# Kernel tuning notes

Hardware: AMD Instinct MI355X
Metric: run time of the kernel (lower is better)

The kernel has to match this reference:

```python
import jax, jax.numpy as jnp
import numpy as np
from jax import lax

NUM_INITS = 64
MODEL_MODE = ['conv', 'conv', 'dense']
SIZE_ARRAY = [(16, 1, 5, 5), (16,), (32, 16, 5, 5), (32,), (10, 512), (10,)]
_flat = [int(np.prod(s)) for s in SIZE_ARRAY]
BP = np.concatenate(([0], np.cumsum(_flat)))  # breakpoints into flat param vector
TOTAL_PARAMS = int(BP[-1])  # 18378
BATCH_N = 128


def setup_inputs() -> dict:
    key = jax.random.key(0)
    k1, k2 = jax.random.split(key)
    params = jax.random.normal(k1, (NUM_INITS, TOTAL_PARAMS), dtype=jnp.float32) * 0.05
    batch = jax.random.normal(k2, (BATCH_N, 1, 28, 28), dtype=jnp.float32)
    return {"params": params, "batch": batch}


def _conv_relu_pool(x, w, b):
    # x: (N, C_in, H, W), w: (C_out, C_in, k, k), b: (C_out,)
    y = lax.conv_general_dilated(x, w, window_strides=(1, 1), padding='VALID',
                                 dimension_numbers=('NCHW', 'OIHW', 'NCHW'))
    y = jax.nn.relu(y + b[None, :, None, None])
    # MaxPool2d(2, 2) over spatial dims
    return lax.reduce_window(y, -jnp.inf, lax.max, (1, 1, 2, 2), (1, 1, 2, 2), 'VALID')


def reference(params, batch):
    # out: (num_inits, N, C, H, W) — ensemble replicated batch
    out = jnp.broadcast_to(batch[None], (NUM_INITS,) + batch.shape)
    i = 0
    for mode in MODEL_MODE:
        w = params[:, BP[i]:BP[i + 1]].reshape((NUM_INITS,) + SIZE_ARRAY[i])
        b = params[:, BP[i + 1]:BP[i + 2]].reshape((NUM_INITS,) + SIZE_ARRAY[i + 1])
        if mode == 'conv':
            # grouped conv over inits == vmap of dense conv over the init axis
            out = jax.vmap(_conv_relu_pool)(out, w, b)
        else:  # dense
            out = out.reshape(out.shape[0], out.shape[1], -1)  # flatten C,H,W
            out = jnp.einsum('inf,iof->ino', out, w) + b[:, None, :]
        i += 2
    return jax.nn.log_softmax(out, axis=2)  # (num_inits, N, 10)
```

## Files before the change

### kernel.cpp

```cpp
#include <hip/hip_runtime.h>
#include <hip/hip_bf16.h>
#include <math.h>

#define P_TOTAL 18378

typedef __attribute__((ext_vector_type(8))) short short8;
typedef __attribute__((ext_vector_type(4))) float float4v;
typedef __attribute__((ext_vector_type(16))) float float16;

__device__ __forceinline__ unsigned short f2bf(float f) {
    union { float f; unsigned u; } v; v.f = f;
    unsigned r = v.u + 0x7fffu + ((v.u >> 16) & 1u);
    return (unsigned short)(r >> 16);
}
__device__ __forceinline__ float bf2f(unsigned short h) {
    union { unsigned u; float f; } v; v.u = ((unsigned)h) << 16;
    return v.f;
}

__global__ __launch_bounds__(256) void prep_kernel(
        const float* __restrict__ params,
        const float* __restrict__ batch,
        unsigned short* __restrict__ wswz,
        unsigned short* __restrict__ w3bf,
        unsigned short* __restrict__ w1bf,
        unsigned short* __restrict__ Bmat) {
    int blk = blockIdx.x;
    int t = threadIdx.x;
    if (blk < 64) {
        int i = blk;
        const float* w2 = params + (size_t)i * P_TOTAL + 416;
        unsigned short* dst = wswz + (size_t)i * 12800;
        for (int k = t; k < 12800; k += 256) {
            int co = k / 400;
            int r = k - co * 400;
            int cin = r / 25;
            int s = r - cin * 25;
            dst[(s * 32 + co) * 16 + cin] = f2bf(w2[k]);
        }
        const float* w3 = params + (size_t)i * P_TOTAL + 13248;
        unsigned short* d3 = w3bf + (size_t)i * 5120;
        for (int k = t; k < 5120; k += 256) d3[k] = f2bf(w3[k]);
        const float* w1 = params + (size_t)i * P_TOTAL;
        unsigned short* d1 = w1bf + (size_t)i * 512;
        for (int e = t; e < 512; e += 256) {
            int m = e >> 5, k = e & 31;
            d1[e] = (k < 25) ? f2bf(w1[m * 25 + k]) : (unsigned short)0;
        }
    } else {
        __shared__ float img[784];
        int j = blk - 64;
        const float* ip = batch + j * 784;
        for (int k = t; k < 784; k += 256) img[k] = ip[k];
        __syncthreads();
        unsigned short* dst = Bmat + (size_t)j * 18432;
        for (int task = t; task < 2304; task += 256) {
            int c = task >> 2, kh = task & 3;
            int pp = c >> 2, q = c & 3;
            int py = pp / 12, px = pp - py * 12;
            int y0 = 2 * py + (q >> 1);
            int x0 = 2 * px + (q & 1);
            unsigned short ov[8] __attribute__((aligned(16)));
#pragma unroll
            for (int u = 0; u < 8; ++u) {
                int k = kh * 8 + u;
                float v = 0.f;
                if (k < 25) {
                    int ky = k / 5, kx = k - ky * 5;
                    v = img[(y0 + ky) * 28 + x0 + kx];
                }
                ov[u] = f2bf(v);
            }
            *(uint4*)(dst + c * 32 + kh * 8) = *(const uint4*)ov;
        }
    }
}

#define A1_PIX_STRIDE 24
#define IMG_LDS (144 * A1_PIX_STRIDE)
__global__ __launch_bounds__(256, 5) void mega_kernel(
        const float* __restrict__ params,
        const unsigned short* __restrict__ Bmat,
        const unsigned short* __restrict__ w1bf,
        const unsigned short* __restrict__ wswz,
        const unsigned short* __restrict__ w3bf,
        float* __restrict__ out) {
    __shared__ unsigned short a1s[4 * IMG_LDS];
    int b = blockIdx.x;
    int i = b >> 5;
    int g = b & 31;
    int t = threadIdx.x;
    int w = t >> 6;
    int lane = t & 63;
    int j = g * 4 + w;

    {
        int co = lane & 15;
        int h4 = lane >> 4;
        short8 wfr = *(const short8*)(w1bf + (size_t)i * 512 + co * 32 + h4 * 8);
        float bias1 = params[(size_t)i * P_TOTAL + 400 + co];
        unsigned short* dst = a1s + w * IMG_LDS;
        const unsigned short* bsrc = Bmat + (size_t)j * 18432;
#pragma unroll 6
        for (int nt = 0; nt < 36; ++nt) {
            short8 afr = *(const short8*)(bsrc + (nt * 16 + co) * 32 + h4 * 8);
            float4v acc = {0.f, 0.f, 0.f, 0.f};
            acc = __builtin_amdgcn_mfma_f32_16x16x32_bf16(afr, wfr, acc, 0, 0, 0);
            float v = fmaxf(fmaxf(acc[0], acc[1]), fmaxf(acc[2], acc[3]));
            v = fmaxf(v + bias1, 0.f);
            dst[(nt * 4 + h4) * A1_PIX_STRIDE + co] = f2bf(v);
        }
    }

    int n = lane & 31;
    int h = lane >> 5;
    const short8* wg = (const short8*)(wswz + (size_t)i * 12800 + n * 16 + h * 8);
    int y0 = n >> 3, x0 = n & 7;
    const unsigned short* bbase = a1s + w * IMG_LDS;
    const short8* bptr0 = (const short8*)(bbase + ((y0    ) * 12 + x0) * A1_PIX_STRIDE + h * 8);
    const short8* bptr1 = (const short8*)(bbase + ((y0 + 4) * 12 + x0) * A1_PIX_STRIDE + h * 8);

    float16 acc0 = {};
    float16 acc1 = {};
#pragma unroll
    for (int ky = 0; ky < 5; ++ky) {
#pragma unroll
        for (int kx = 0; kx < 5; ++kx) {
            int tap = ky * 5 + kx;
            short8 af = wg[tap * 64];
            int bo = (ky * 12 + kx) * 3;
            short8 b0 = bptr0[bo];
            short8 b1 = bptr1[bo];
            acc0 = __builtin_amdgcn_mfma_f32_32x32x16_bf16(af, b0, acc0, 0, 0, 0);
            acc1 = __builtin_amdgcn_mfma_f32_32x32x16_bf16(af, b1, acc1, 0, 0, 0);
        }
    }

    float* sw = (float*)(a1s + w * IMG_LDS);
    int co2 = lane >> 1;
    int half = lane & 1;
    float bias2 = params[(size_t)i * P_TOTAL + 13216 + co2];
    float xr[8];

#pragma unroll
    for (int r = 0; r < 16; ++r) {
        int co = (r & 3) + 8 * (r >> 2) + 4 * h;
        sw[co * 33 + n] = acc0[r];
    }
    if (half == 0) {
#pragma unroll
        for (int it = 0; it < 8; ++it) {
            int py = it >> 2, px = it & 3;
            const float* s = sw + co2 * 33 + (py * 2) * 8 + px * 2;
            float v = fmaxf(fmaxf(s[0], s[1]), fmaxf(s[8], s[9]));
            xr[it] = fmaxf(v + bias2, 0.f);
        }
    }
#pragma unroll
    for (int r = 0; r < 16; ++r) {
        int co = (r & 3) + 8 * (r >> 2) + 4 * h;
        sw[co * 33 + n] = acc1[r];
    }
    if (half == 1) {
#pragma unroll
        for (int it = 0; it < 8; ++it) {
            int pyl = it >> 2, px = it & 3;
            const float* s = sw + co2 * 33 + (pyl * 2) * 8 + px * 2;
            float v = fmaxf(fmaxf(s[0], s[1]), fmaxf(s[8], s[9]));
            xr[it] = fmaxf(v + bias2, 0.f);
        }
    }

    const unsigned short* w3p = w3bf + (size_t)i * 5120 + lane * 8;
    float acc[10];
#pragma unroll
    for (int o = 0; o < 10; ++o) {
        uint4 u = *(const uint4*)(w3p + o * 512);
        float a = 0.f;
        a = fmaf(xr[0], bf2f((unsigned short)(u.x & 0xffffu)), a);
        a = fmaf(xr[1], bf2f((unsigned short)(u.x >> 16)), a);
        a = fmaf(xr[2], bf2f((unsigned short)(u.y & 0xffffu)), a);
        a = fmaf(xr[3], bf2f((unsigned short)(u.y >> 16)), a);
        a = fmaf(xr[4], bf2f((unsigned short)(u.z & 0xffffu)), a);
        a = fmaf(xr[5], bf2f((unsigned short)(u.z >> 16)), a);
        a = fmaf(xr[6], bf2f((unsigned short)(u.w & 0xffffu)), a);
        a = fmaf(xr[7], bf2f((unsigned short)(u.w >> 16)), a);
#pragma unroll
        for (int d = 32; d >= 1; d >>= 1) a += __shfl_xor(a, d, 64);
        acc[o] = a;
    }
    const float* bp = params + (size_t)i * P_TOTAL + 18368;
    float m = -3.4e38f;
#pragma unroll
    for (int o = 0; o < 10; ++o) { acc[o] += bp[o]; m = fmaxf(m, acc[o]); }
    float ssum = 0.f;
#pragma unroll
    for (int o = 0; o < 10; ++o) ssum += expf(acc[o] - m);
    float ls = logf(ssum) + m;
    if (lane == 0) {
        float* op = out + ((size_t)i * 128 + j) * 10;
#pragma unroll
        for (int o = 0; o < 10; ++o) op[o] = acc[o] - ls;
    }
}

extern "C" void kernel_launch(void* const* d_in, const int* in_sizes, int n_in,
                              void* d_out, int out_size, void* d_ws, size_t ws_size,
                              hipStream_t stream) {
    const float* params = (const float*)d_in[0];
    const float* batch  = (const float*)d_in[1];
    float* out = (float*)d_out;

    unsigned short* wswz = (unsigned short*)d_ws;
    unsigned short* w3bf = wswz + (size_t)64 * 12800;
    unsigned short* w1bf = w3bf + (size_t)64 * 5120;
    unsigned short* Bmat = w1bf + (size_t)64 * 512;

    prep_kernel<<<192, 256, 0, stream>>>(params, batch, wswz, w3bf, w1bf, Bmat);
    mega_kernel<<<2048, 256, 0, stream>>>(params, Bmat, w1bf, wswz, w3bf, out);
}
```

Before: 107.8 us.

## Transpose conv2 MFMA operands so pooling happens in registers

Swaps the A/B operands of the conv2 MFMA so each lane's accumulator holds spatial pixels for a single output channel. The 2x2 max-pool is then done directly on accumulator registers, removing the LDS round trip through a scratch buffer. The dense-layer weights are pre-permuted in the prep kernel to match the new per-lane feature ordering. This depends on the MFMA output layout mapping exactly onto the pool windows and the permuted weight order, and a mismatch would silently give wrong results.

After: 106.8 us. Within noise of the previous version (-0.9%).

```diff
diff --git a/kernel.cpp b/kernel.cpp
--- a/kernel.cpp
+++ b/kernel.cpp
@@ -22,7 +22,7 @@
         const float* __restrict__ params,
         const float* __restrict__ batch,
         unsigned short* __restrict__ wswz,
-        unsigned short* __restrict__ w3bf,
+        unsigned short* __restrict__ w3l,
         unsigned short* __restrict__ w1bf,
         unsigned short* __restrict__ Bmat) {
     int blk = blockIdx.x;
@@ -39,8 +39,14 @@
             dst[(s * 32 + co) * 16 + cin] = f2bf(w2[k]);
         }
         const float* w3 = params + (size_t)i * P_TOTAL + 13248;
-        unsigned short* d3 = w3bf + (size_t)i * 5120;
-        for (int k = t; k < 5120; k += 256) d3[k] = f2bf(w3[k]);
+        unsigned short* d3 = w3l + (size_t)i * 5120;
+        for (int k = t; k < 5120; k += 256) {
+            int o = k >> 9, r = k & 511;
+            int l = r >> 3, s = r & 7;
+            int co = l & 31, h = l >> 5;
+            int py = s >> 1, d = s & 1;
+            d3[k] = f2bf(w3[o * 512 + co * 16 + py * 4 + 2 * h + d]);
+        }
         const float* w1 = params + (size_t)i * P_TOTAL;
         unsigned short* d1 = w1bf + (size_t)i * 512;
         for (int e = t; e < 512; e += 256) {
@@ -83,7 +89,7 @@
         const unsigned short* __restrict__ Bmat,
         const unsigned short* __restrict__ w1bf,
         const unsigned short* __restrict__ wswz,
-        const unsigned short* __restrict__ w3bf,
+        const unsigned short* __restrict__ w3l,
         float* __restrict__ out) {
     __shared__ unsigned short a1s[4 * IMG_LDS];
     int b = blockIdx.x;
@@ -117,8 +123,8 @@
     const short8* wg = (const short8*)(wswz + (size_t)i * 12800 + n * 16 + h * 8);
     int y0 = n >> 3, x0 = n & 7;
     const unsigned short* bbase = a1s + w * IMG_LDS;
-    const short8* bptr0 = (const short8*)(bbase + ((y0    ) * 12 + x0) * A1_PIX_STRIDE + h * 8);
-    const short8* bptr1 = (const short8*)(bbase + ((y0 + 4) * 12 + x0) * A1_PIX_STRIDE + h * 8);
+    const short8* pptr0 = (const short8*)(bbase + ((y0    ) * 12 + x0) * A1_PIX_STRIDE + h * 8);
+    const short8* pptr1 = (const short8*)(bbase + ((y0 + 4) * 12 + x0) * A1_PIX_STRIDE + h * 8);
 
     float16 acc0 = {};
     float16 acc1 = {};
@@ -127,51 +133,33 @@
 #pragma unroll
         for (int kx = 0; kx < 5; ++kx) {
             int tap = ky * 5 + kx;
-            short8 af = wg[tap * 64];
+            short8 wf = wg[tap * 64];
             int bo = (ky * 12 + kx) * 3;
-            short8 b0 = bptr0[bo];
-            short8 b1 = bptr1[bo];
-            acc0 = __builtin_amdgcn_mfma_f32_32x32x16_bf16(af, b0, acc0, 0, 0, 0);
-            acc1 = __builtin_amdgcn_mfma_f32_32x32x16_bf16(af, b1, acc1, 0, 0, 0);
-        }
-    }
-
-    float* sw = (float*)(a1s + w * IMG_LDS);
-    int co2 = lane >> 1;
-    int half = lane & 1;
+            short8 p0 = pptr0[bo];
+            short8 p1 = pptr1[bo];
+            acc0 = __builtin_amdgcn_mfma_f32_32x32x16_bf16(p0, wf, acc0, 0, 0, 0);
+            acc1 = __builtin_amdgcn_mfma_f32_32x32x16_bf16(p1, wf, acc1, 0, 0, 0);
+        }
+    }
+
+    int co2 = lane & 31;
     float bias2 = params[(size_t)i * P_TOTAL + 13216 + co2];
     float xr[8];
-
-#pragma unroll
-    for (int r = 0; r < 16; ++r) {
-        int co = (r & 3) + 8 * (r >> 2) + 4 * h;
-        sw[co * 33 + n] = acc0[r];
-    }
-    if (half == 0) {
-#pragma unroll
-        for (int it = 0; it < 8; ++it) {
-            int py = it >> 2, px = it & 3;
-            const float* s = sw + co2 * 33 + (py * 2) * 8 + px * 2;
-            float v = fmaxf(fmaxf(s[0], s[1]), fmaxf(s[8], s[9]));
-            xr[it] = fmaxf(v + bias2, 0.f);
-        }
-    }
-#pragma unroll
-    for (int r = 0; r < 16; ++r) {
-        int co = (r & 3) + 8 * (r >> 2) + 4 * h;
-        sw[co * 33 + n] = acc1[r];
-    }
-    if (half == 1) {
-#pragma unroll
-        for (int it = 0; it < 8; ++it) {
-            int pyl = it >> 2, px = it & 3;
-            const float* s = sw + co2 * 33 + (pyl * 2) * 8 + px * 2;
-            float v = fmaxf(fmaxf(s[0], s[1]), fmaxf(s[8], s[9]));
-            xr[it] = fmaxf(v + bias2, 0.f);
-        }
-    }
-
-    const unsigned short* w3p = w3bf + (size_t)i * 5120 + lane * 8;
+#pragma unroll
+    for (int pyl = 0; pyl < 2; ++pyl) {
+#pragma unroll
+        for (int d = 0; d < 2; ++d) {
+            int base = pyl * 8 + d * 2;
+            float v0 = fmaxf(fmaxf(acc0[base], acc0[base + 1]),
+                             fmaxf(acc0[base + 4], acc0[base + 5]));
+            float v1 = fmaxf(fmaxf(acc1[base], acc1[base + 1]),
+                             fmaxf(acc1[base + 4], acc1[base + 5]));
+            xr[pyl * 2 + d]     = fmaxf(v0 + bias2, 0.f);
+            xr[4 + pyl * 2 + d] = fmaxf(v1 + bias2, 0.f);
+        }
+    }
+
+    const unsigned short* w3p = w3l + (size_t)i * 5120 + lane * 8;
     float acc[10];
 #pragma unroll
     for (int o = 0; o < 10; ++o) {
@@ -212,10 +200,10 @@
     float* out = (float*)d_out;
 
     unsigned short* wswz = (unsigned short*)d_ws;
-    unsigned short* w3bf = wswz + (size_t)64 * 12800;
-    unsigned short* w1bf = w3bf + (size_t)64 * 5120;
+    unsigned short* w3l  = wswz + (size_t)64 * 12800;
+    unsigned short* w1bf = w3l + (size_t)64 * 5120;
     unsigned short* Bmat = w1bf + (size_t)64 * 512;
 
-    prep_kernel<<<192, 256, 0, stream>>>(params, batch, wswz, w3bf, w1bf, Bmat);
-    mega_kernel<<<2048, 256, 0, stream>>>(params, Bmat, w1bf, wswz, w3bf, out);
-}
+    prep_kernel<<<192, 256, 0, stream>>>(params, batch, wswz, w3l, w1bf, Bmat);
+    mega_kernel<<<2048, 256, 0, stream>>>(params, Bmat, w1bf, wswz, w3l, out);
+}
```
